# Performance work log

Hardware: AMD Instinct MI355X
Metric: run time of the kernel (lower is better)

## Reference

```python
import jax, jax.numpy as jnp
import numpy as np

FIN = 4096
N_MEM = 256
SQRT_FIN = 64  # int(FIN ** 0.5)


def setup_inputs() -> dict:
    key = jax.random.key(0)
    ks = jax.random.split(key, 6)
    scale = 0.02  # keep relu-relu scores numerically tame
    x = jax.random.normal(ks[0], (1024, FIN), dtype=jnp.float32)
    Wq = jax.random.normal(ks[1], (FIN, SQRT_FIN * N_MEM), dtype=jnp.float32) * scale
    bq = jnp.zeros((SQRT_FIN * N_MEM,), dtype=jnp.float32)
    Wk = jax.random.normal(ks[2], (FIN, SQRT_FIN * N_MEM), dtype=jnp.float32) * scale
    bk = jnp.zeros((SQRT_FIN * N_MEM,), dtype=jnp.float32)
    v = jax.random.normal(ks[3], (N_MEM, FIN), dtype=jnp.float32) * scale
    Wl = jax.random.normal(ks[4], (FIN, FIN), dtype=jnp.float32) * scale
    bl = jnp.zeros((FIN,), dtype=jnp.float32)
    return {"x": x, "Wq": Wq, "bq": bq, "Wk": Wk, "bk": bk, "v": v, "Wl": Wl, "bl": bl}


def reference(x, Wq, bq, Wk, bk, v, Wl, bl):
    B = x.shape[0]
    # Q/K projections, reshaped to [B, n_mem, sqrt_fin]
    xq = (x @ Wq + bq).reshape(B, N_MEM, SQRT_FIN)
    xk = (x @ Wk + bk).reshape(B, N_MEM, SQRT_FIN)
    # relu-relu score matrix [B, n_mem, n_mem], scaled by sqrt(sqrt_fin)
    scores = jnp.einsum('bms,bns->bmn', jax.nn.relu(xq), jax.nn.relu(xk))
    scores = scores / jnp.sqrt(jnp.asarray(SQRT_FIN, dtype=x.dtype))
    # multiply by learned value memory v [n_mem, fin] (broadcast over batch)
    mem = jnp.einsum('bmn,nf->bmf', scores, v)
    # mean over memory slots, output projection, residual
    pooled = mem.mean(axis=1)  # [B, fin]
    return x + (pooled @ Wl + bl)
```

## Files before the change

kernel.cpp:

```cpp
#include <hip/hip_runtime.h>
#include <hip/hip_bf16.h>
#include <stdint.h>

#define B_SZ 1024
#define FIN  4096
#define NMEM 256
#define NQK  16384

typedef __attribute__((ext_vector_type(8))) short short8;
typedef __attribute__((ext_vector_type(4))) float floatx4;

__device__ __forceinline__ ushort f2bf(float f) {
    uint32_t u = __float_as_uint(f);
    return (ushort)((u + 0x7fffu + ((u >> 16) & 1u)) >> 16);
}
__device__ __forceinline__ float bf2f(ushort u) {
    return __uint_as_float(((uint32_t)u) << 16);
}

__device__ __forceinline__ void gl2lds16(const void* g, void* l) {
    __builtin_amdgcn_global_load_lds(
        (const __attribute__((address_space(1))) void*)g,
        (__attribute__((address_space(3))) void*)l, 16, 0, 0);
}

__global__ void cvt_kernel(const float* __restrict__ src, ushort* __restrict__ dst, int n) {
    int i = (blockIdx.x * blockDim.x + threadIdx.x) * 8;
    if (i >= n) return;
    float4 f0 = *(const float4*)(src + i);
    float4 f1 = *(const float4*)(src + i + 4);
    uint4 o;
    o.x = (uint32_t)f2bf(f0.x) | ((uint32_t)f2bf(f0.y) << 16);
    o.y = (uint32_t)f2bf(f0.z) | ((uint32_t)f2bf(f0.w) << 16);
    o.z = (uint32_t)f2bf(f1.x) | ((uint32_t)f2bf(f1.y) << 16);
    o.w = (uint32_t)f2bf(f1.z) | ((uint32_t)f2bf(f1.w) << 16);
    *(uint4*)(dst + i) = o;
}

__global__ __launch_bounds__(256)
void transT_kernel(const float* __restrict__ src, ushort* __restrict__ dst,
                   int NFULL, int n0) {
    __shared__ float lds[64 * 65];
    const int tid = threadIdx.x;
    const int nc0 = blockIdx.x * 64;
    const int k0  = blockIdx.y * 64;
    #pragma unroll
    for (int p = 0; p < 4; ++p) {
        int idx = p * 256 + tid;
        int krow = idx >> 4;
        int c4 = (idx & 15) * 4;
        float4 v = *(const float4*)(src + (size_t)(k0 + krow) * NFULL + n0 + nc0 + c4);
        lds[krow * 65 + c4 + 0] = v.x;
        lds[krow * 65 + c4 + 1] = v.y;
        lds[krow * 65 + c4 + 2] = v.z;
        lds[krow * 65 + c4 + 3] = v.w;
    }
    __syncthreads();
    #pragma unroll
    for (int p = 0; p < 2; ++p) {
        int idx = p * 256 + tid;
        int nrow = idx >> 3;
        int c8 = (idx & 7) * 8;
        ushort t[8];
        #pragma unroll
        for (int j = 0; j < 8; ++j) t[j] = f2bf(lds[(c8 + j) * 65 + nrow]);
        uint4 o;
        o.x = (uint32_t)t[0] | ((uint32_t)t[1] << 16);
        o.y = (uint32_t)t[2] | ((uint32_t)t[3] << 16);
        o.z = (uint32_t)t[4] | ((uint32_t)t[5] << 16);
        o.w = (uint32_t)t[6] | ((uint32_t)t[7] << 16);
        *(uint4*)(dst + (size_t)(nc0 + nrow) * 4096 + k0 + c8) = o;
    }
}

template<int RELU, int HASBIAS>
__global__ __launch_bounds__(512, 2)
void gemm256(const ushort* __restrict__ A, const ushort* __restrict__ Bt,
             const float* __restrict__ bias, ushort* __restrict__ C,
             int ldc, int K)
{
    __shared__ __align__(16) ushort As[2][256 * 64];
    __shared__ __align__(16) ushort Bs[2][256 * 64];

    const int tid  = threadIdx.x;
    const int lane = tid & 63;
    const int wave = tid >> 6;
    const int wr   = wave >> 2;
    const int wc   = wave & 3;
    const int m0 = blockIdx.y * 256;
    const int n0 = blockIdx.x * 256;
    const int fr = lane & 15;
    const int fq = lane >> 4;
    const int NT = K >> 6;

    floatx4 acc[8][4] = {};
    short8 a_[4][2];
    short8 b0_[2][2];
    short8 b1_[2][2];

    auto stage_half = [&](const ushort* __restrict__ G, int grow0, ushort* L,
                          int h, int k0) {
        #pragma unroll
        for (int i = 0; i < 2; ++i) {
            int id  = i * 512 + tid;
            int row = h * 128 + (id >> 3);
            int pos = id & 7;
            int cc  = pos ^ (row & 7);
            gl2lds16(G + (size_t)(grow0 + row) * K + k0 + cc * 8,
                     L + h * 8192 + (i * 512 + wave * 64) * 8);
        }
    };

#define LOAD_A(QM)                                                             \
    {                                                                          \
        _Pragma("unroll")                                                      \
        for (int j = 0; j < 4; ++j) {                                          \
            int r = wr * 128 + ((QM) * 4 + j) * 16 + fr;                       \
            _Pragma("unroll")                                                  \
            for (int ks = 0; ks < 2; ++ks) {                                   \
                int p = (ks * 4 + fq) ^ (r & 7);                               \
                a_[j][ks] = *(const short8*)(&Acur[r * 64 + p * 8]);           \
            }                                                                  \
        }                                                                      \
    }

#define LOAD_B(QN, BB)                                                         \
    {                                                                          \
        _Pragma("unroll")                                                      \
        for (int j = 0; j < 2; ++j) {                                          \
            int r = wc * 64 + ((QN) * 2 + j) * 16 + fr;                        \
            _Pragma("unroll")                                                  \
            for (int ks = 0; ks < 2; ++ks) {                                   \
                int p = (ks * 4 + fq) ^ (r & 7);                               \
                BB[j][ks] = *(const short8*)(&Bcur[r * 64 + p * 8]);           \
            }                                                                  \
        }                                                                      \
    }

#define MFMA_CL(QM, QN, BB)                                                    \
    __builtin_amdgcn_s_setprio(1);                                             \
    _Pragma("unroll")                                                          \
    for (int ks = 0; ks < 2; ++ks)                                             \
        _Pragma("unroll")                                                      \
        for (int j = 0; j < 4; ++j)                                            \
            _Pragma("unroll")                                                  \
            for (int i = 0; i < 2; ++i)                                        \
                acc[(QM) * 4 + j][(QN) * 2 + i] =                              \
                    __builtin_amdgcn_mfma_f32_16x16x32_bf16(                   \
                        a_[j][ks], BB[i][ks],                                  \
                        acc[(QM) * 4 + j][(QN) * 2 + i], 0, 0, 0);             \
    __builtin_amdgcn_s_setprio(0);

    stage_half(A,  m0, &As[0][0], 0, 0);
    stage_half(A,  m0, &As[0][0], 1, 0);
    stage_half(Bt, n0, &Bs[0][0], 0, 0);
    stage_half(Bt, n0, &Bs[0][0], 1, 0);

    for (int kt = 0; kt < NT - 1; ++kt) {
        const int cur = kt & 1;
        const ushort* Acur = &As[cur][0];
        const ushort* Bcur = &Bs[cur][0];
        ushort* An = &As[cur ^ 1][0];
        ushort* Bn = &Bs[cur ^ 1][0];
        const int k0n = (kt + 1) << 6;

        stage_half(A, m0, An, 0, k0n);
        asm volatile("s_waitcnt vmcnt(2)" ::: "memory");
        __builtin_amdgcn_s_barrier();
        __builtin_amdgcn_sched_barrier(0);
        LOAD_A(0);
        LOAD_B(0, b0_);
        asm volatile("s_waitcnt lgkmcnt(0)" ::: "memory");
        __builtin_amdgcn_sched_barrier(0);
        MFMA_CL(0, 0, b0_);
        __builtin_amdgcn_s_barrier();

        LOAD_B(1, b1_);
        stage_half(A, m0, An, 1, k0n);
        __builtin_amdgcn_s_barrier();
        asm volatile("s_waitcnt lgkmcnt(0)" ::: "memory");
        __builtin_amdgcn_sched_barrier(0);
        MFMA_CL(0, 1, b1_);
        __builtin_amdgcn_s_barrier();

        LOAD_A(1);
        stage_half(Bt, n0, Bn, 0, k0n);
        __builtin_amdgcn_s_barrier();
        asm volatile("s_waitcnt lgkmcnt(0)" ::: "memory");
        __builtin_amdgcn_sched_barrier(0);
        MFMA_CL(1, 0, b0_);
        __builtin_amdgcn_s_barrier();

        stage_half(Bt, n0, Bn, 1, k0n);
        __builtin_amdgcn_s_barrier();
        MFMA_CL(1, 1, b1_);
        __builtin_amdgcn_s_barrier();
    }

    {
        const ushort* Acur = &As[(NT - 1) & 1][0];
        const ushort* Bcur = &Bs[(NT - 1) & 1][0];
        asm volatile("s_waitcnt vmcnt(0)" ::: "memory");
        __builtin_amdgcn_s_barrier();
        __builtin_amdgcn_sched_barrier(0);
        LOAD_A(0);
        LOAD_B(0, b0_);
        LOAD_B(1, b1_);
        MFMA_CL(0, 0, b0_);
        MFMA_CL(0, 1, b1_);
        LOAD_A(1);
        MFMA_CL(1, 0, b0_);
        MFMA_CL(1, 1, b1_);
    }

    #pragma unroll
    for (int mi = 0; mi < 8; ++mi) {
        #pragma unroll
        for (int ni = 0; ni < 4; ++ni) {
            #pragma unroll
            for (int r = 0; r < 4; ++r) {
                int gm = m0 + wr * 128 + mi * 16 + fq * 4 + r;
                int gn = n0 + wc * 64 + ni * 16 + fr;
                float val = acc[mi][ni][r];
                if (HASBIAS) val += bias[gn];
                if (RELU)    val = fmaxf(val, 0.0f);
                C[(size_t)gm * ldc + gn] = f2bf(val);
            }
        }
    }
#undef LOAD_A
#undef LOAD_B
#undef MFMA_CL
}

template<int RELU, int HASBIAS, int RESID, int OUTBF>
__global__ __launch_bounds__(256)
void gemm_bf(const ushort* __restrict__ A, const ushort* __restrict__ Bt,
             const float* __restrict__ bias, const float* __restrict__ resid,
             void* __restrict__ Cout, int ldc, int M, int K)
{
    __shared__ __align__(16) ushort As[128 * 64];
    __shared__ __align__(16) ushort Bs[128 * 64];

    const int tid  = threadIdx.x;
    const int lane = tid & 63;
    const int wave = tid >> 6;
    const int wm = (wave >> 1) * 64;
    const int wn = (wave & 1) * 64;
    const int m0 = blockIdx.y * 128;
    const int n0 = blockIdx.x * 128;

    const int fr = lane & 15;
    const int fq = lane >> 4;

    floatx4 acc[4][4] = {};

    for (int k0 = 0; k0 < K; k0 += 64) {
        __syncthreads();
        #pragma unroll
        for (int i = 0; i < 4; ++i) {
            int id = i * 256 + wave * 64 + lane;
            int row = id >> 3, pos = id & 7;
            int c = pos ^ (row & 7);
            gl2lds16(A + (size_t)(m0 + row) * K + k0 + c * 8,
                     &As[(i * 256 + wave * 64) * 8]);
        }
        #pragma unroll
        for (int i = 0; i < 4; ++i) {
            int id = i * 256 + wave * 64 + lane;
            int row = id >> 3, pos = id & 7;
            int c = pos ^ (row & 7);
            gl2lds16(Bt + (size_t)(n0 + row) * K + k0 + c * 8,
                     &Bs[(i * 256 + wave * 64) * 8]);
        }
        __syncthreads();

        #pragma unroll
        for (int ks = 0; ks < 2; ++ks) {
            short8 a[4], b[4];
            #pragma unroll
            for (int i = 0; i < 4; ++i) {
                int row = wm + i * 16 + fr;
                int p = (ks * 4 + fq) ^ (row & 7);
                a[i] = *(const short8*)(&As[row * 64 + p * 8]);
            }
            #pragma unroll
            for (int i = 0; i < 4; ++i) {
                int row = wn + i * 16 + fr;
                int p = (ks * 4 + fq) ^ (row & 7);
                b[i] = *(const short8*)(&Bs[row * 64 + p * 8]);
            }
            #pragma unroll
            for (int mi = 0; mi < 4; ++mi)
                #pragma unroll
                for (int ni = 0; ni < 4; ++ni)
                    acc[mi][ni] = __builtin_amdgcn_mfma_f32_16x16x32_bf16(
                        a[mi], b[ni], acc[mi][ni], 0, 0, 0);
        }
    }

    #pragma unroll
    for (int mi = 0; mi < 4; ++mi) {
        #pragma unroll
        for (int ni = 0; ni < 4; ++ni) {
            #pragma unroll
            for (int r = 0; r < 4; ++r) {
                int gm = m0 + wm + mi * 16 + fq * 4 + r;
                int gn = n0 + wn + ni * 16 + fr;
                float val = acc[mi][ni][r];
                if (HASBIAS) val += bias[gn];
                if (RELU)    val = fmaxf(val, 0.0f);
                if (RESID)   val += resid[(size_t)gm * ldc + gn];
                if (OUTBF) ((ushort*)Cout)[(size_t)gm * ldc + gn] = f2bf(val);
                else       ((float*)Cout)[(size_t)gm * ldc + gn] = val;
            }
        }
    }
}

#define BM 128
#define BN 128
#define BKK 64
#define LDA 72
#define LDB 72

template<int RELU, int HASBIAS, int RESID, int OUTBF>
__global__ __launch_bounds__(256)
void gemm_k(const ushort* __restrict__ A, const float* __restrict__ B,
            const float* __restrict__ bias, const float* __restrict__ resid,
            void* __restrict__ Cout, int M, int N, int K)
{
    __shared__ ushort As[BM * LDA];
    __shared__ ushort Bs[BN * LDB];

    const int tid  = threadIdx.x;
    const int lane = tid & 63;
    const int wave = tid >> 6;
    const int wm = (wave >> 1) * 64;
    const int wn = (wave & 1) * 64;
    const int m0 = blockIdx.y * BM;
    const int n0 = blockIdx.x * BN;

    const int fr = lane & 15;
    const int fq = lane >> 4;

    floatx4 acc[4][4] = {};

    for (int k0 = 0; k0 < K; k0 += BKK) {
        __syncthreads();
        #pragma unroll
        for (int c = 0; c < 4; ++c) {
            int idx = c * 256 + tid;
            int row = idx >> 3;
            int off = idx & 7;
            *(uint4*)(&As[row * LDA + off * 8]) =
                *(const uint4*)(A + (size_t)(m0 + row) * K + k0 + off * 8);
        }
        #pragma unroll
        for (int p = 0; p < 8; ++p) {
            int idx = p * 256 + tid;
            int nn = idx & 127;
            int kg = idx >> 7;
            const float* bp = B + (size_t)(k0 + kg * 4) * N + n0 + nn;
            float f0 = bp[0];
            float f1 = bp[N];
            float f2 = bp[2 * (size_t)N];
            float f3 = bp[3 * (size_t)N];
            ushort4 w;
            w.x = f2bf(f0); w.y = f2bf(f1); w.z = f2bf(f2); w.w = f2bf(f3);
            *(ushort4*)(&Bs[nn * LDB + kg * 4]) = w;
        }
        __syncthreads();

        #pragma unroll
        for (int ks = 0; ks < 2; ++ks) {
            short8 a[4], b[4];
            #pragma unroll
            for (int i = 0; i < 4; ++i)
                a[i] = *(const short8*)(&As[(wm + i * 16 + fr) * LDA + ks * 32 + fq * 8]);
            #pragma unroll
            for (int i = 0; i < 4; ++i)
                b[i] = *(const short8*)(&Bs[(wn + i * 16 + fr) * LDB + ks * 32 + fq * 8]);
            #pragma unroll
            for (int mi = 0; mi < 4; ++mi)
                #pragma unroll
                for (int ni = 0; ni < 4; ++ni)
                    acc[mi][ni] = __builtin_amdgcn_mfma_f32_16x16x32_bf16(
                        a[mi], b[ni], acc[mi][ni], 0, 0, 0);
        }
    }

    #pragma unroll
    for (int mi = 0; mi < 4; ++mi) {
        #pragma unroll
        for (int ni = 0; ni < 4; ++ni) {
            #pragma unroll
            for (int r = 0; r < 4; ++r) {
                int gm = m0 + wm + mi * 16 + fq * 4 + r;
                int gn = n0 + wn + ni * 16 + fr;
                float val = acc[mi][ni][r];
                if (HASBIAS) val += bias[gn];
                if (RELU)    val = fmaxf(val, 0.0f);
                if (RESID)   val += resid[(size_t)gm * N + gn];
                if (OUTBF) ((ushort*)Cout)[(size_t)gm * N + gn] = f2bf(val);
                else       ((float*)Cout)[(size_t)gm * N + gn] = val;
            }
        }
    }
}

__global__ void qbar_kernel(const ushort* __restrict__ XQr, float* __restrict__ qbar) {
    int b = blockIdx.x;
    int s = threadIdx.x;
    const ushort* p = XQr + (size_t)b * NQK + s;
    float sum = 0.0f;
    #pragma unroll 4
    for (int m = 0; m < NMEM; ++m) sum += bf2f(p[m * 64]);
    qbar[b * 64 + s] = sum * (1.0f / (NMEM * 8.0f));
}

__global__ void spool_kernel(const ushort* __restrict__ XKr, const float* __restrict__ qbar,
                             ushort* __restrict__ spb) {
    int b = blockIdx.x;
    int n = threadIdx.x;
    __shared__ float q[64];
    if (threadIdx.x < 64) q[threadIdx.x] = qbar[b * 64 + threadIdx.x];
    __syncthreads();
    const ushort* p = XKr + (size_t)b * NQK + n * 64;
    float sum = 0.0f;
    #pragma unroll
    for (int s = 0; s < 64; s += 4) {
        ushort4 u = *(const ushort4*)(p + s);
        sum += bf2f(u.x) * q[s] + bf2f(u.y) * q[s + 1]
             + bf2f(u.z) * q[s + 2] + bf2f(u.w) * q[s + 3];
    }
    spb[b * 256 + n] = f2bf(sum);
}

extern "C" void kernel_launch(void* const* d_in, const int* in_sizes, int n_in,
                              void* d_out, int out_size, void* d_ws, size_t ws_size,
                              hipStream_t stream) {
    const float* x  = (const float*)d_in[0];
    const float* Wq = (const float*)d_in[1];
    const float* bq = (const float*)d_in[2];
    const float* Wk = (const float*)d_in[3];
    const float* bk = (const float*)d_in[4];
    const float* v  = (const float*)d_in[5];
    const float* Wl = (const float*)d_in[6];
    const float* bl = (const float*)d_in[7];
    float* out = (float*)d_out;

    const size_t MB = 1ull << 20;
    char* ws = (char*)d_ws;
    ushort* xb   = (ushort*)(ws + 0);
    ushort* XQr  = (ushort*)(ws + 8 * MB);
    ushort* XKr  = (ushort*)(ws + 40 * MB);
    float*  qbar = (float*)(ws + 72 * MB);
    ushort* spb  = (ushort*)(ws + 73 * MB);
    ushort* p2b  = (ushort*)(ws + 74 * MB);
    ushort* WT   = (ushort*)(ws + 82 * MB);

    cvt_kernel<<<dim3((B_SZ * FIN) / 8 / 256), 256, 0, stream>>>(x, xb, B_SZ * FIN);

    transT_kernel<<<dim3(NQK / 64, FIN / 64), 256, 0, stream>>>(Wq, WT, NQK, 0);
    gemm256<1, 1><<<dim3(NQK / 256, B_SZ / 256), 512, 0, stream>>>(
        xb, WT, bq, XQr, NQK, FIN);
    qbar_kernel<<<dim3(B_SZ), 64, 0, stream>>>(XQr, qbar);

    transT_kernel<<<dim3(NQK / 64, FIN / 64), 256, 0, stream>>>(Wk, WT, NQK, 0);
    gemm256<1, 1><<<dim3(NQK / 256, B_SZ / 256), 512, 0, stream>>>(
        xb, WT, bk, XKr, NQK, FIN);
    spool_kernel<<<dim3(B_SZ), 256, 0, stream>>>(XKr, qbar, spb);

    gemm_k<0, 0, 0, 1><<<dim3(FIN / BN, B_SZ / BM), 256, 0, stream>>>(
        spb, v, nullptr, nullptr, p2b, B_SZ, FIN, NMEM);

    transT_kernel<<<dim3(FIN / 64, FIN / 64), 256, 0, stream>>>(Wl, WT, FIN, 0);
    gemm_bf<0, 1, 1, 0><<<dim3(FIN / 128, B_SZ / 128), 256, 0, stream>>>(
        p2b, WT, bl, x, out, FIN, B_SZ, FIN);
}
```

Baseline: 1.049 ms.

## Restructure GEMM k-loop to prefetch A half two tiles ahead

Reorders the double-buffered staging schedule so the first half of the A tile for iteration k+2 is issued into the current buffer after its last LDS read. The remaining halves for k+1 are spread across the earlier MFMA clusters. This removes the peeled epilogue iteration and one barrier per iteration, giving global loads more lead time before the vmcnt wait. It adds conditional staging branches and relies on the current A buffer being fully read into registers before it is overwritten, which is a subtle race risk.

```diff
diff --git a/kernel.cpp b/kernel.cpp
--- a/kernel.cpp
+++ b/kernel.cpp
@@ -155,28 +155,32 @@
     stage_half(A,  m0, &As[0][0], 1, 0);
     stage_half(Bt, n0, &Bs[0][0], 0, 0);
     stage_half(Bt, n0, &Bs[0][0], 1, 0);
-
-    for (int kt = 0; kt < NT - 1; ++kt) {
+    stage_half(A,  m0, &As[1][0], 0, 64);
+    asm volatile("s_waitcnt vmcnt(2)" ::: "memory");
+    __builtin_amdgcn_s_barrier();
+
+    for (int kt = 0; kt < NT; ++kt) {
         const int cur = kt & 1;
         const ushort* Acur = &As[cur][0];
         const ushort* Bcur = &Bs[cur][0];
+        ushort* Abuf = &As[cur][0];
         ushort* An = &As[cur ^ 1][0];
         ushort* Bn = &Bs[cur ^ 1][0];
-        const int k0n = (kt + 1) << 6;
-
-        stage_half(A, m0, An, 0, k0n);
-        asm volatile("s_waitcnt vmcnt(2)" ::: "memory");
-        __builtin_amdgcn_s_barrier();
-        __builtin_amdgcn_sched_barrier(0);
+        const int k1 = (kt + 1) << 6;
+        const int k2 = (kt + 2) << 6;
+        const bool stg1 = kt + 1 < NT;
+        const bool stg2 = kt + 2 < NT;
+
         LOAD_A(0);
         LOAD_B(0, b0_);
+        if (stg1) stage_half(A, m0, An, 1, k1);
         asm volatile("s_waitcnt lgkmcnt(0)" ::: "memory");
         __builtin_amdgcn_sched_barrier(0);
         MFMA_CL(0, 0, b0_);
         __builtin_amdgcn_s_barrier();
 
         LOAD_B(1, b1_);
-        stage_half(A, m0, An, 1, k0n);
+        if (stg1) stage_half(Bt, n0, Bn, 0, k1);
         __builtin_amdgcn_s_barrier();
         asm volatile("s_waitcnt lgkmcnt(0)" ::: "memory");
         __builtin_amdgcn_sched_barrier(0);
@@ -184,33 +188,20 @@
         __builtin_amdgcn_s_barrier();
 
         LOAD_A(1);
-        stage_half(Bt, n0, Bn, 0, k0n);
+        if (stg1) stage_half(Bt, n0, Bn, 1, k1);
         __builtin_amdgcn_s_barrier();
         asm volatile("s_waitcnt lgkmcnt(0)" ::: "memory");
         __builtin_amdgcn_sched_barrier(0);
         MFMA_CL(1, 0, b0_);
         __builtin_amdgcn_s_barrier();
 
-        stage_half(Bt, n0, Bn, 1, k0n);
-        __builtin_amdgcn_s_barrier();
+        if (stg2) stage_half(A, m0, Abuf, 0, k2);
         MFMA_CL(1, 1, b1_);
-        __builtin_amdgcn_s_barrier();
-    }
-
-    {
-        const ushort* Acur = &As[(NT - 1) & 1][0];
-        const ushort* Bcur = &Bs[(NT - 1) & 1][0];
-        asm volatile("s_waitcnt vmcnt(0)" ::: "memory");
-        __builtin_amdgcn_s_barrier();
-        __builtin_amdgcn_sched_barrier(0);
-        LOAD_A(0);
-        LOAD_B(0, b0_);
-        LOAD_B(1, b1_);
-        MFMA_CL(0, 0, b0_);
-        MFMA_CL(0, 1, b1_);
-        LOAD_A(1);
-        MFMA_CL(1, 0, b0_);
-        MFMA_CL(1, 1, b1_);
+        if (kt < NT - 1) {
+            if (stg2) { asm volatile("s_waitcnt vmcnt(2)" ::: "memory"); }
+            else      { asm volatile("s_waitcnt vmcnt(0)" ::: "memory"); }
+            __builtin_amdgcn_s_barrier();
+        }
     }
 
     #pragma unroll
```

Result: faster. 1.009 ms (-3.8%).
